# Kernel tuning notes

Measured on AMD Instinct MI355X. Metric: run time of the kernel, lower is better.

## Reference

```python
import jax, jax.numpy as jnp
import numpy as np


def setup_inputs() -> dict:
    key = jax.random.key(0)
    k1, k2, k3 = jax.random.split(key, 3)
    B, S, dk = 8, 4096, 64  # per-head tensors; dk = embedding_size / h = 1024 / 16
    q = jax.random.normal(k1, (B, S, dk), dtype=jnp.float32)
    k = jax.random.normal(k2, (B, S, dk), dtype=jnp.float32)
    v = jax.random.normal(k3, (B, S, dk), dtype=jnp.float32)
    return {"q": q, "k": k, "v": v}


def reference(q, k, v):
    dk = q.shape[-1]
    # QK = q @ k^T scaled by 1/dk (NOT 1/sqrt(dk) -- faithful to source)
    scores = jnp.einsum("bqd,bkd->bqk", q, k) / dk  # [B, S, S]
    # padding mask derived from exact-zero score entries: -inf where QK == 0
    pad_mask = jnp.where(scores == 0, -jnp.inf, 0.0)
    # look-ahead (causal) mask: 0 where i >= j else -inf
    S = scores.shape[-1]
    causal = jnp.where(
        jnp.arange(S)[:, None] >= jnp.arange(S)[None, :], 0.0, -jnp.inf
    )  # [S, S]
    scores = scores + pad_mask + causal
    attn = jax.nn.softmax(scores, axis=-1)
    # NaN cleanup for fully-masked rows (softmax over all -inf)
    attn = jnp.where(jnp.isnan(attn), 0.0, attn)
    return jnp.einsum("bqk,bkd->bqd", attn, v)
```

## Files before the change

kernel.cpp:

```cpp
#include <hip/hip_runtime.h>
#include <hip/hip_bf16.h>
#include <stdint.h>

#define S_LEN 4096
#define DK    64
#define BQ    64
#define BK    64

typedef __bf16 bf16x8  __attribute__((ext_vector_type(8)));
typedef float  f32x16  __attribute__((ext_vector_type(16)));

__device__ __forceinline__ short f2bf(float f) {
    union { __bf16 h; short s; } u; u.h = (__bf16)f; return u.s;
}
__device__ __forceinline__ short4 cvt4(float4 f) {
    short4 s; s.x = f2bf(f.x); s.y = f2bf(f.y); s.z = f2bf(f.z); s.w = f2bf(f.w); return s;
}

__device__ __forceinline__ uint32_t cvtpk_bf16(float lo, float hi) {
    uint32_t d;
    asm("v_cvt_pk_bf16_f32 %0, %1, %2" : "=&v"(d) : "v"(lo), "v"(hi));
    return d;
}
__device__ __forceinline__ void plswap(uint32_t& a, uint32_t& b) {
    asm("v_permlane32_swap_b32 %0, %1" : "+v"(a), "+v"(b));
}

__device__ __forceinline__ void gload_lds16(const void* g, void* l) {
    auto gp = reinterpret_cast<const uint32_t __attribute__((address_space(1)))*>(
        reinterpret_cast<uintptr_t>(g));
    auto lp = reinterpret_cast<uint32_t __attribute__((address_space(3)))*>(
        reinterpret_cast<uintptr_t>(l));
    __builtin_amdgcn_global_load_lds(gp, lp, 16, 0, 0);
}

__device__ __forceinline__ int swz(int row) {
    return ((row ^ (row >> 3)) & 7) << 3;
}

__global__ __launch_bounds__(256) void prep_kernel(
    const float* __restrict__ K, const float* __restrict__ V,
    short* __restrict__ WK, short* __restrict__ WV)
{
    const int t = blockIdx.x, b = blockIdx.y;
    const int tid = threadIdx.x;
    const size_t ibase = ((size_t)b * S_LEN + (size_t)t * 64) * DK;
    const size_t obase = ((size_t)b * 64 + t) * 4096;
    const int r0 = tid >> 4;
    const int c0 = (tid & 15) * 4;

    #pragma unroll
    for (int i = 0; i < 4; ++i) {
        const int row = r0 + 16 * i;
        const float4 f = *reinterpret_cast<const float4*>(K + ibase + (size_t)row * DK + c0);
        *reinterpret_cast<short4*>(WK + obase + row * 64 + (c0 ^ swz(row))) = cvt4(f);
    }
    float4 vf[4];
    #pragma unroll
    for (int j = 0; j < 4; ++j)
        vf[j] = *reinterpret_cast<const float4*>(V + ibase + (size_t)(4 * r0 + j) * DK + c0);
    #pragma unroll
    for (int jj = 0; jj < 4; ++jj) {
        const int d = c0 + jj;
        short4 sp;
        sp.x = f2bf(reinterpret_cast<const float*>(&vf[0])[jj]);
        sp.y = f2bf(reinterpret_cast<const float*>(&vf[1])[jj]);
        sp.z = f2bf(reinterpret_cast<const float*>(&vf[2])[jj]);
        sp.w = f2bf(reinterpret_cast<const float*>(&vf[3])[jj]);
        *reinterpret_cast<short4*>(WV + obase + d * 64 + ((4 * r0) ^ swz(d))) = sp;
    }
}

__global__ __launch_bounds__(512, 2) void attn_kernel(
    const float* __restrict__ Q, float* __restrict__ O,
    const short* __restrict__ WK, const short* __restrict__ WV)
{
    __shared__ __align__(16) short Ks[2][16384];
    __shared__ __align__(16) short Vts[2][16384];
    __shared__ float2 Ml[4][2][32];

    const int tid  = threadIdx.x;
    const int wave = tid >> 6;
    const int lane = tid & 63;
    const int q32  = lane & 31;
    const int hi   = lane >> 5;
    const int hi4  = hi * 4;
    const int hi8  = hi * 8;
    const int grp  = wave & 3;
    const int qsub = wave >> 2;

    const int batch = blockIdx.y;
    const size_t bo = (size_t)batch * S_LEN * DK;
    const short* WKb = WK + (size_t)batch * 262144;
    const short* WVb = WV + (size_t)batch * 262144;

    auto stage_quad = [&](int quad, int buf) {
        const char* gk = (const char*)(WKb + (size_t)quad * 16384) + wave * 1024 + lane * 16;
        const char* gv = (const char*)(WVb + (size_t)quad * 16384) + wave * 1024 + lane * 16;
        char* lk = (char*)(&Ks[buf][0]) + wave * 1024;
        char* lv = (char*)(&Vts[buf][0]) + wave * 1024;
        #pragma unroll
        for (int i = 0; i < 4; ++i) {
            gload_lds16(gk + i * 8192, lk + i * 8192);
            gload_lds16(gv + i * 8192, lv + i * 8192);
        }
    };

    const float NEG_INF = -__builtin_inff();
    const float QSCALE  = 0.015625f * 1.44269504088896341f;
    const float THR     = 8.0f;
    const int swz0 = swz(q32);
    const int swz1 = swz(32 + q32);

    #pragma unroll 1
    for (int qi = 0; qi < 2; ++qi) {
        const int qb = qi ? (int)blockIdx.x : 63 - (int)blockIdx.x;
        const int q0 = qb * BQ;
        const int ntiles = qb + 1;
        const int nquads = (ntiles + 3) >> 2;
        const int qrow   = q0 + 32 * qsub + q32;

        bf16x8 qf[4];
        {
            const float* Qr = Q + bo + (size_t)qrow * DK;
            #pragma unroll
            for (int s = 0; s < 4; ++s) {
                const float4 a = *reinterpret_cast<const float4*>(Qr + 16 * s + hi8);
                const float4 b = *reinterpret_cast<const float4*>(Qr + 16 * s + hi8 + 4);
                qf[s][0] = (__bf16)(a.x * QSCALE); qf[s][1] = (__bf16)(a.y * QSCALE);
                qf[s][2] = (__bf16)(a.z * QSCALE); qf[s][3] = (__bf16)(a.w * QSCALE);
                qf[s][4] = (__bf16)(b.x * QSCALE); qf[s][5] = (__bf16)(b.y * QSCALE);
                qf[s][6] = (__bf16)(b.z * QSCALE); qf[s][7] = (__bf16)(b.w * QSCALE);
            }
        }

        float m_run = NEG_INF, l_run = 0.f;
        f32x16 oa0, oa1;
        #pragma unroll
        for (int r = 0; r < 16; ++r) { oa0[r] = 0.f; oa1[r] = 0.f; }

        stage_quad(0, 0);
        __syncthreads();

        for (int p = 0; p < nquads; ++p) {
            const int kt = 4 * p + grp;
            const bool pf = (p + 1 < nquads);
            if (pf) stage_quad(p + 1, (p + 1) & 1);

            const short* Kt = &Ks[p & 1][grp * 4096];
            const short* Vt = &Vts[p & 1][grp * 4096];
            const bool act = (kt < ntiles);

            if (act) {
                f32x16 sa0, sa1;
                #pragma unroll
                for (int r = 0; r < 16; ++r) { sa0[r] = 0.f; sa1[r] = 0.f; }
                __builtin_amdgcn_s_setprio(1);
                #pragma unroll
                for (int s = 0; s < 4; ++s) {
                    const int col = 16 * s + hi8;
                    const bf16x8 kf0 = *reinterpret_cast<const bf16x8*>(&Kt[q32 * 64 + (col ^ swz0)]);
                    const bf16x8 kf1 = *reinterpret_cast<const bf16x8*>(&Kt[(32 + q32) * 64 + (col ^ swz1)]);
                    sa0 = __builtin_amdgcn_mfma_f32_32x32x16_bf16(kf0, qf[s], sa0, 0, 0, 0);
                    sa1 = __builtin_amdgcn_mfma_f32_32x32x16_bf16(kf1, qf[s], sa1, 0, 0, 0);
                }
                __builtin_amdgcn_s_setprio(0);

                float ma[4] = {NEG_INF, NEG_INF, NEG_INF, NEG_INF};
                if (kt == qb) {
                    const int keybase = kt * BK + hi4;
                    #pragma unroll
                    for (int r = 0; r < 16; ++r) {
                        const int kl = (r & 3) + 8 * (r >> 2);
                        if (keybase + kl > qrow) sa0[r] = NEG_INF;
                        ma[r & 3] = fmaxf(ma[r & 3], sa0[r]);
                        if (keybase + kl + 32 > qrow) sa1[r] = NEG_INF;
                        ma[r & 3] = fmaxf(ma[r & 3], sa1[r]);
                    }
                } else {
                    #pragma unroll
                    for (int r = 0; r < 16; ++r) {
                        ma[r & 3] = fmaxf(ma[r & 3], sa0[r]);
                        ma[r & 3] = fmaxf(ma[r & 3], sa1[r]);
                    }
                }
                float mt = fmaxf(fmaxf(ma[0], ma[1]), fmaxf(ma[2], ma[3]));
                mt = fmaxf(mt, __shfl_xor(mt, 32));

                if (!__all(mt <= m_run + THR)) {
                    const float mnew = fmaxf(m_run, mt);
                    const float alpha = __builtin_amdgcn_exp2f(m_run - mnew);
                    m_run = mnew;
                    l_run *= alpha;
                    #pragma unroll
                    for (int r = 0; r < 16; ++r) {
                        const float ar = __shfl(alpha, (r & 3) + 8 * (r >> 2) + hi4);
                        oa0[r] *= ar; oa1[r] *= ar;
                    }
                }

                float pp[4] = {0.f, 0.f, 0.f, 0.f};
                #pragma unroll
                for (int r = 0; r < 16; ++r) {
                    sa0[r] = __builtin_amdgcn_exp2f(sa0[r] - m_run); pp[r & 3] += sa0[r];
                    sa1[r] = __builtin_amdgcn_exp2f(sa1[r] - m_run); pp[r & 3] += sa1[r];
                }
                float ps = (pp[0] + pp[1]) + (pp[2] + pp[3]);
                ps += __shfl_xor(ps, 32);
                l_run += ps;

                __builtin_amdgcn_s_setprio(1);
                #pragma unroll
                for (int c = 0; c < 2; ++c) {
                    const f32x16& sp = c ? sa1 : sa0;
                    #pragma unroll
                    for (int s2 = 0; s2 < 2; ++s2) {
                        uint32_t a0 = cvtpk_bf16(sp[8*s2+0], sp[8*s2+1]);
                        uint32_t a1 = cvtpk_bf16(sp[8*s2+2], sp[8*s2+3]);
                        uint32_t b0 = cvtpk_bf16(sp[8*s2+4], sp[8*s2+5]);
                        uint32_t b1 = cvtpk_bf16(sp[8*s2+6], sp[8*s2+7]);
                        plswap(a0, b0);
                        plswap(a1, b1);
                        union { uint32_t u[4]; bf16x8 v; } pw;
                        pw.u[0] = a0; pw.u[1] = a1; pw.u[2] = b0; pw.u[3] = b1;
                        const int vcol = 32 * c + 16 * s2 + hi8;
                        const bf16x8 vf0 = *reinterpret_cast<const bf16x8*>(&Vt[q32 * 64 + (vcol ^ swz0)]);
                        const bf16x8 vf1 = *reinterpret_cast<const bf16x8*>(&Vt[(32 + q32) * 64 + (vcol ^ swz1)]);
                        oa0 = __builtin_amdgcn_mfma_f32_32x32x16_bf16(pw.v, vf0, oa0, 0, 0, 0);
                        oa1 = __builtin_amdgcn_mfma_f32_32x32x16_bf16(pw.v, vf1, oa1, 0, 0, 0);
                    }
                }
                __builtin_amdgcn_s_setprio(0);
            }

            __syncthreads();
        }

        if (hi == 0) Ml[grp][qsub][q32] = make_float2(m_run, l_run);
        float4* Om4 = reinterpret_cast<float4*>(&Ks[0][0]);
        if (grp != 0) {
            const int midx = (grp - 1) * 2 + qsub;
            #pragma unroll
            for (int c = 0; c < 2; ++c)
                #pragma unroll
                for (int rq = 0; rq < 4; ++rq) {
                    float4 ov;
                    if (c == 0) { ov.x = oa0[4*rq]; ov.y = oa0[4*rq+1]; ov.z = oa0[4*rq+2]; ov.w = oa0[4*rq+3]; }
                    else        { ov.x = oa1[4*rq]; ov.y = oa1[4*rq+1]; ov.z = oa1[4*rq+2]; ov.w = oa1[4*rq+3]; }
                    Om4[(midx * 8 + c * 4 + rq) * 64 + lane] = ov;
                }
        }
        __syncthreads();
        if (grp == 0) {
            const float* Omf = reinterpret_cast<const float*>(&Ks[0][0]);
            float* Ob = O + bo;
            #pragma unroll
            for (int r = 0; r < 16; ++r) {
                const int row_r = (r & 3) + 8 * (r >> 2) + hi4;
                float mg[4], lg[4];
                #pragma unroll
                for (int g = 0; g < 4; ++g) {
                    const float2 v = Ml[g][qsub][row_r];
                    mg[g] = v.x; lg[g] = v.y;
                }
                const float mtot = fmaxf(fmaxf(mg[0], mg[1]), fmaxf(mg[2], mg[3]));
                float eg[4], ltot = 0.f;
                #pragma unroll
                for (int g = 0; g < 4; ++g) {
                    eg[g] = (mg[g] == NEG_INF) ? 0.f : __builtin_amdgcn_exp2f(mg[g] - mtot);
                    ltot += eg[g] * lg[g];
                }
                const float inv = (ltot > 0.f) ? (1.0f / ltot) : 0.f;
                #pragma unroll
                for (int c = 0; c < 2; ++c) {
                    float acc = eg[0] * ((c == 0) ? oa0[r] : oa1[r]);
                    #pragma unroll
                    for (int g = 1; g < 4; ++g) {
                        const int midx = (g - 1) * 2 + qsub;
                        acc += eg[g] * Omf[((midx * 8 + c * 4 + (r >> 2)) * 64 + lane) * 4 + (r & 3)];
                    }
                    Ob[(size_t)(q0 + 32 * qsub + row_r) * DK + 32 * c + q32] = acc * inv;
                }
            }
        }
        __syncthreads();
    }
}

extern "C" void kernel_launch(void* const* d_in, const int* in_sizes, int n_in,
                              void* d_out, int out_size, void* d_ws, size_t ws_size,
                              hipStream_t stream) {
    (void)in_sizes; (void)n_in; (void)out_size; (void)ws_size;
    const float* q = (const float*)d_in[0];
    const float* k = (const float*)d_in[1];
    const float* v = (const float*)d_in[2];
    float* o = (float*)d_out;
    short* wk = (short*)d_ws;
    short* wv = wk + (size_t)8 * 64 * 4096;

    hipLaunchKernelGGL(prep_kernel, dim3(64, 8), dim3(256), 0, stream, k, v, wk, wv);
    hipLaunchKernelGGL(attn_kernel, dim3(32, 8), dim3(512), 0, stream, q, o, wk, wv);
}
```

Measured before the change: 53.37 us.

## Replace LDS-staged split-K attention with single-wave blocks reading fragments from global

The attention kernel becomes one 64-thread wave per 32 query rows. Each wave walks every causal key tile itself, loading K/V MFMA fragments straight from global memory in a new fragment-major layout written by the prep kernel. This removes LDS staging, the barriers and the cross-wave softmax merge, and launches 1024 small blocks. In exchange K/V reuse across waves now relies on the L2 cache instead of LDS. Per-wave work is no longer balanced across the causal triangle, and global-load latency is exposed without a software pipeline.

Measured after the change: 71.10 us. 1.33x slower.

```diff
diff --git a/kernel.cpp b/kernel.cpp
--- a/kernel.cpp
+++ b/kernel.cpp
@@ -4,17 +4,12 @@
 
 #define S_LEN 4096
 #define DK    64
-#define BQ    64
-#define BK    64
 
 typedef __bf16 bf16x8  __attribute__((ext_vector_type(8)));
 typedef float  f32x16  __attribute__((ext_vector_type(16)));
 
 __device__ __forceinline__ short f2bf(float f) {
     union { __bf16 h; short s; } u; u.h = (__bf16)f; return u.s;
-}
-__device__ __forceinline__ short4 cvt4(float4 f) {
-    short4 s; s.x = f2bf(f.x); s.y = f2bf(f.y); s.z = f2bf(f.z); s.w = f2bf(f.w); return s;
 }
 
 __device__ __forceinline__ uint32_t cvtpk_bf16(float lo, float hi) {
@@ -24,18 +19,6 @@
 }
 __device__ __forceinline__ void plswap(uint32_t& a, uint32_t& b) {
     asm("v_permlane32_swap_b32 %0, %1" : "+v"(a), "+v"(b));
-}
-
-__device__ __forceinline__ void gload_lds16(const void* g, void* l) {
-    auto gp = reinterpret_cast<const uint32_t __attribute__((address_space(1)))*>(
-        reinterpret_cast<uintptr_t>(g));
-    auto lp = reinterpret_cast<uint32_t __attribute__((address_space(3)))*>(
-        reinterpret_cast<uintptr_t>(l));
-    __builtin_amdgcn_global_load_lds(gp, lp, 16, 0, 0);
-}
-
-__device__ __forceinline__ int swz(int row) {
-    return ((row ^ (row >> 3)) & 7) << 3;
 }
 
 __global__ __launch_bounds__(256) void prep_kernel(
@@ -49,241 +32,180 @@
     const int r0 = tid >> 4;
     const int c0 = (tid & 15) * 4;
 
-    #pragma unroll
-    for (int i = 0; i < 4; ++i) {
-        const int row = r0 + 16 * i;
-        const float4 f = *reinterpret_cast<const float4*>(K + ibase + (size_t)row * DK + c0);
-        *reinterpret_cast<short4*>(WK + obase + row * 64 + (c0 ^ swz(row))) = cvt4(f);
-    }
-    float4 vf[4];
-    #pragma unroll
-    for (int j = 0; j < 4; ++j)
-        vf[j] = *reinterpret_cast<const float4*>(V + ibase + (size_t)(4 * r0 + j) * DK + c0);
-    #pragma unroll
-    for (int jj = 0; jj < 4; ++jj) {
-        const int d = c0 + jj;
-        short4 sp;
-        sp.x = f2bf(reinterpret_cast<const float*>(&vf[0])[jj]);
-        sp.y = f2bf(reinterpret_cast<const float*>(&vf[1])[jj]);
-        sp.z = f2bf(reinterpret_cast<const float*>(&vf[2])[jj]);
-        sp.w = f2bf(reinterpret_cast<const float*>(&vf[3])[jj]);
-        *reinterpret_cast<short4*>(WV + obase + d * 64 + ((4 * r0) ^ swz(d))) = sp;
-    }
-}
-
-__global__ __launch_bounds__(512, 2) void attn_kernel(
+    {
+        const int s = c0 >> 4, h = (c0 >> 3) & 1, e = c0 & 7;
+        #pragma unroll
+        for (int i = 0; i < 4; ++i) {
+            const int row = r0 + 16 * i;
+            const float4 f = *reinterpret_cast<const float4*>(K + ibase + (size_t)row * DK + c0);
+            short4 sp;
+            sp.x = f2bf(f.x); sp.y = f2bf(f.y); sp.z = f2bf(f.z); sp.w = f2bf(f.w);
+            *reinterpret_cast<short4*>(WK + obase + (size_t)s * 1024 + (row * 2 + h) * 8 + e) = sp;
+        }
+    }
+    {
+        float4 vf[4];
+        #pragma unroll
+        for (int j = 0; j < 4; ++j)
+            vf[j] = *reinterpret_cast<const float4*>(V + ibase + (size_t)(4 * r0 + j) * DK + c0);
+        const int sk = r0 >> 2, hk = (r0 >> 1) & 1, ek = (r0 & 1) * 4;
+        #pragma unroll
+        for (int jj = 0; jj < 4; ++jj) {
+            const int d = c0 + jj;
+            short4 sp;
+            sp.x = f2bf(reinterpret_cast<const float*>(&vf[0])[jj]);
+            sp.y = f2bf(reinterpret_cast<const float*>(&vf[1])[jj]);
+            sp.z = f2bf(reinterpret_cast<const float*>(&vf[2])[jj]);
+            sp.w = f2bf(reinterpret_cast<const float*>(&vf[3])[jj]);
+            *reinterpret_cast<short4*>(WV + obase + (size_t)sk * 1024 + (d * 2 + hk) * 8 + ek) = sp;
+        }
+    }
+}
+
+__global__ __launch_bounds__(64, 2) void attn_kernel(
     const float* __restrict__ Q, float* __restrict__ O,
     const short* __restrict__ WK, const short* __restrict__ WV)
 {
-    __shared__ __align__(16) short Ks[2][16384];
-    __shared__ __align__(16) short Vts[2][16384];
-    __shared__ float2 Ml[4][2][32];
-
-    const int tid  = threadIdx.x;
-    const int wave = tid >> 6;
-    const int lane = tid & 63;
+    const int lane = threadIdx.x;
     const int q32  = lane & 31;
     const int hi   = lane >> 5;
     const int hi4  = hi * 4;
     const int hi8  = hi * 8;
-    const int grp  = wave & 3;
-    const int qsub = wave >> 2;
 
     const int batch = blockIdx.y;
+    const int qb    = 63 - ((int)blockIdx.x >> 1);
+    const int qsub  = blockIdx.x & 1;
     const size_t bo = (size_t)batch * S_LEN * DK;
     const short* WKb = WK + (size_t)batch * 262144;
     const short* WVb = WV + (size_t)batch * 262144;
 
-    auto stage_quad = [&](int quad, int buf) {
-        const char* gk = (const char*)(WKb + (size_t)quad * 16384) + wave * 1024 + lane * 16;
-        const char* gv = (const char*)(WVb + (size_t)quad * 16384) + wave * 1024 + lane * 16;
-        char* lk = (char*)(&Ks[buf][0]) + wave * 1024;
-        char* lv = (char*)(&Vts[buf][0]) + wave * 1024;
-        #pragma unroll
-        for (int i = 0; i < 4; ++i) {
-            gload_lds16(gk + i * 8192, lk + i * 8192);
-            gload_lds16(gv + i * 8192, lv + i * 8192);
-        }
-    };
+    const int q0   = qb * 64;
+    const int qrow = q0 + 32 * qsub + q32;
+    const int idx8 = (q32 * 2 + hi) * 8;
 
     const float NEG_INF = -__builtin_inff();
+    const float MFLOOR  = -1e38f;
     const float QSCALE  = 0.015625f * 1.44269504088896341f;
     const float THR     = 8.0f;
-    const int swz0 = swz(q32);
-    const int swz1 = swz(32 + q32);
-
-    #pragma unroll 1
-    for (int qi = 0; qi < 2; ++qi) {
-        const int qb = qi ? (int)blockIdx.x : 63 - (int)blockIdx.x;
-        const int q0 = qb * BQ;
-        const int ntiles = qb + 1;
-        const int nquads = (ntiles + 3) >> 2;
-        const int qrow   = q0 + 32 * qsub + q32;
-
-        bf16x8 qf[4];
-        {
-            const float* Qr = Q + bo + (size_t)qrow * DK;
-            #pragma unroll
-            for (int s = 0; s < 4; ++s) {
-                const float4 a = *reinterpret_cast<const float4*>(Qr + 16 * s + hi8);
-                const float4 b = *reinterpret_cast<const float4*>(Qr + 16 * s + hi8 + 4);
-                qf[s][0] = (__bf16)(a.x * QSCALE); qf[s][1] = (__bf16)(a.y * QSCALE);
-                qf[s][2] = (__bf16)(a.z * QSCALE); qf[s][3] = (__bf16)(a.w * QSCALE);
-                qf[s][4] = (__bf16)(b.x * QSCALE); qf[s][5] = (__bf16)(b.y * QSCALE);
-                qf[s][6] = (__bf16)(b.z * QSCALE); qf[s][7] = (__bf16)(b.w * QSCALE);
-            }
-        }
-
-        float m_run = NEG_INF, l_run = 0.f;
-        f32x16 oa0, oa1;
-        #pragma unroll
-        for (int r = 0; r < 16; ++r) { oa0[r] = 0.f; oa1[r] = 0.f; }
-
-        stage_quad(0, 0);
-        __syncthreads();
-
-        for (int p = 0; p < nquads; ++p) {
-            const int kt = 4 * p + grp;
-            const bool pf = (p + 1 < nquads);
-            if (pf) stage_quad(p + 1, (p + 1) & 1);
-
-            const short* Kt = &Ks[p & 1][grp * 4096];
-            const short* Vt = &Vts[p & 1][grp * 4096];
-            const bool act = (kt < ntiles);
-
-            if (act) {
-                f32x16 sa0, sa1;
-                #pragma unroll
-                for (int r = 0; r < 16; ++r) { sa0[r] = 0.f; sa1[r] = 0.f; }
-                __builtin_amdgcn_s_setprio(1);
-                #pragma unroll
-                for (int s = 0; s < 4; ++s) {
-                    const int col = 16 * s + hi8;
-                    const bf16x8 kf0 = *reinterpret_cast<const bf16x8*>(&Kt[q32 * 64 + (col ^ swz0)]);
-                    const bf16x8 kf1 = *reinterpret_cast<const bf16x8*>(&Kt[(32 + q32) * 64 + (col ^ swz1)]);
-                    sa0 = __builtin_amdgcn_mfma_f32_32x32x16_bf16(kf0, qf[s], sa0, 0, 0, 0);
-                    sa1 = __builtin_amdgcn_mfma_f32_32x32x16_bf16(kf1, qf[s], sa1, 0, 0, 0);
-                }
-                __builtin_amdgcn_s_setprio(0);
-
-                float ma[4] = {NEG_INF, NEG_INF, NEG_INF, NEG_INF};
-                if (kt == qb) {
-                    const int keybase = kt * BK + hi4;
-                    #pragma unroll
-                    for (int r = 0; r < 16; ++r) {
-                        const int kl = (r & 3) + 8 * (r >> 2);
-                        if (keybase + kl > qrow) sa0[r] = NEG_INF;
-                        ma[r & 3] = fmaxf(ma[r & 3], sa0[r]);
-                        if (keybase + kl + 32 > qrow) sa1[r] = NEG_INF;
-                        ma[r & 3] = fmaxf(ma[r & 3], sa1[r]);
-                    }
-                } else {
-                    #pragma unroll
-                    for (int r = 0; r < 16; ++r) {
-                        ma[r & 3] = fmaxf(ma[r & 3], sa0[r]);
-                        ma[r & 3] = fmaxf(ma[r & 3], sa1[r]);
-                    }
-                }
-                float mt = fmaxf(fmaxf(ma[0], ma[1]), fmaxf(ma[2], ma[3]));
-                mt = fmaxf(mt, __shfl_xor(mt, 32));
-
-                if (!__all(mt <= m_run + THR)) {
-                    const float mnew = fmaxf(m_run, mt);
-                    const float alpha = __builtin_amdgcn_exp2f(m_run - mnew);
-                    m_run = mnew;
-                    l_run *= alpha;
-                    #pragma unroll
-                    for (int r = 0; r < 16; ++r) {
-                        const float ar = __shfl(alpha, (r & 3) + 8 * (r >> 2) + hi4);
-                        oa0[r] *= ar; oa1[r] *= ar;
-                    }
-                }
-
-                float pp[4] = {0.f, 0.f, 0.f, 0.f};
-                #pragma unroll
-                for (int r = 0; r < 16; ++r) {
-                    sa0[r] = __builtin_amdgcn_exp2f(sa0[r] - m_run); pp[r & 3] += sa0[r];
-                    sa1[r] = __builtin_amdgcn_exp2f(sa1[r] - m_run); pp[r & 3] += sa1[r];
-                }
-                float ps = (pp[0] + pp[1]) + (pp[2] + pp[3]);
-                ps += __shfl_xor(ps, 32);
-                l_run += ps;
-
-                __builtin_amdgcn_s_setprio(1);
-                #pragma unroll
-                for (int c = 0; c < 2; ++c) {
-                    const f32x16& sp = c ? sa1 : sa0;
-                    #pragma unroll
-                    for (int s2 = 0; s2 < 2; ++s2) {
-                        uint32_t a0 = cvtpk_bf16(sp[8*s2+0], sp[8*s2+1]);
-                        uint32_t a1 = cvtpk_bf16(sp[8*s2+2], sp[8*s2+3]);
-                        uint32_t b0 = cvtpk_bf16(sp[8*s2+4], sp[8*s2+5]);
-                        uint32_t b1 = cvtpk_bf16(sp[8*s2+6], sp[8*s2+7]);
-                        plswap(a0, b0);
-                        plswap(a1, b1);
-                        union { uint32_t u[4]; bf16x8 v; } pw;
-                        pw.u[0] = a0; pw.u[1] = a1; pw.u[2] = b0; pw.u[3] = b1;
-                        const int vcol = 32 * c + 16 * s2 + hi8;
-                        const bf16x8 vf0 = *reinterpret_cast<const bf16x8*>(&Vt[q32 * 64 + (vcol ^ swz0)]);
-                        const bf16x8 vf1 = *reinterpret_cast<const bf16x8*>(&Vt[(32 + q32) * 64 + (vcol ^ swz1)]);
-                        oa0 = __builtin_amdgcn_mfma_f32_32x32x16_bf16(pw.v, vf0, oa0, 0, 0, 0);
-                        oa1 = __builtin_amdgcn_mfma_f32_32x32x16_bf16(pw.v, vf1, oa1, 0, 0, 0);
-                    }
-                }
-                __builtin_amdgcn_s_setprio(0);
-            }
-
-            __syncthreads();
-        }
-
-        if (hi == 0) Ml[grp][qsub][q32] = make_float2(m_run, l_run);
-        float4* Om4 = reinterpret_cast<float4*>(&Ks[0][0]);
-        if (grp != 0) {
-            const int midx = (grp - 1) * 2 + qsub;
-            #pragma unroll
-            for (int c = 0; c < 2; ++c)
-                #pragma unroll
-                for (int rq = 0; rq < 4; ++rq) {
-                    float4 ov;
-                    if (c == 0) { ov.x = oa0[4*rq]; ov.y = oa0[4*rq+1]; ov.z = oa0[4*rq+2]; ov.w = oa0[4*rq+3]; }
-                    else        { ov.x = oa1[4*rq]; ov.y = oa1[4*rq+1]; ov.z = oa1[4*rq+2]; ov.w = oa1[4*rq+3]; }
-                    Om4[(midx * 8 + c * 4 + rq) * 64 + lane] = ov;
-                }
-        }
-        __syncthreads();
-        if (grp == 0) {
-            const float* Omf = reinterpret_cast<const float*>(&Ks[0][0]);
-            float* Ob = O + bo;
+
+    bf16x8 qf[4];
+    {
+        const float* Qr = Q + bo + (size_t)qrow * DK;
+        #pragma unroll
+        for (int s = 0; s < 4; ++s) {
+            const float4 a = *reinterpret_cast<const float4*>(Qr + 16 * s + hi8);
+            const float4 b = *reinterpret_cast<const float4*>(Qr + 16 * s + hi8 + 4);
+            qf[s][0] = (__bf16)(a.x * QSCALE); qf[s][1] = (__bf16)(a.y * QSCALE);
+            qf[s][2] = (__bf16)(a.z * QSCALE); qf[s][3] = (__bf16)(a.w * QSCALE);
+            qf[s][4] = (__bf16)(b.x * QSCALE); qf[s][5] = (__bf16)(b.y * QSCALE);
+            qf[s][6] = (__bf16)(b.z * QSCALE); qf[s][7] = (__bf16)(b.w * QSCALE);
+        }
+    }
+
+    float m_run = MFLOOR, l_run = 0.f;
+    f32x16 oa0, oa1;
+    #pragma unroll
+    for (int r = 0; r < 16; ++r) { oa0[r] = 0.f; oa1[r] = 0.f; }
+
+    for (int kt = 0; kt <= qb; ++kt) {
+        const short* Kt = WKb + (size_t)kt * 4096;
+        const short* Vt = WVb + (size_t)kt * 4096;
+
+        bf16x8 kf0[4], kf1[4], vf0[4], vf1[4];
+        #pragma unroll
+        for (int s = 0; s < 4; ++s) {
+            kf0[s] = *reinterpret_cast<const bf16x8*>(Kt + s * 1024 + idx8);
+            kf1[s] = *reinterpret_cast<const bf16x8*>(Kt + s * 1024 + 512 + idx8);
+        }
+        #pragma unroll
+        for (int s = 0; s < 4; ++s) {
+            vf0[s] = *reinterpret_cast<const bf16x8*>(Vt + s * 1024 + idx8);
+            vf1[s] = *reinterpret_cast<const bf16x8*>(Vt + s * 1024 + 512 + idx8);
+        }
+
+        f32x16 sa0, sa1;
+        #pragma unroll
+        for (int r = 0; r < 16; ++r) { sa0[r] = 0.f; sa1[r] = 0.f; }
+        __builtin_amdgcn_s_setprio(1);
+        #pragma unroll
+        for (int s = 0; s < 4; ++s) {
+            sa0 = __builtin_amdgcn_mfma_f32_32x32x16_bf16(kf0[s], qf[s], sa0, 0, 0, 0);
+            sa1 = __builtin_amdgcn_mfma_f32_32x32x16_bf16(kf1[s], qf[s], sa1, 0, 0, 0);
+        }
+        __builtin_amdgcn_s_setprio(0);
+
+        float ma[4] = {NEG_INF, NEG_INF, NEG_INF, NEG_INF};
+        if (kt == qb) {
+            const int keybase = kt * 64 + hi4;
             #pragma unroll
             for (int r = 0; r < 16; ++r) {
-                const int row_r = (r & 3) + 8 * (r >> 2) + hi4;
-                float mg[4], lg[4];
-                #pragma unroll
-                for (int g = 0; g < 4; ++g) {
-                    const float2 v = Ml[g][qsub][row_r];
-                    mg[g] = v.x; lg[g] = v.y;
-                }
-                const float mtot = fmaxf(fmaxf(mg[0], mg[1]), fmaxf(mg[2], mg[3]));
-                float eg[4], ltot = 0.f;
-                #pragma unroll
-                for (int g = 0; g < 4; ++g) {
-                    eg[g] = (mg[g] == NEG_INF) ? 0.f : __builtin_amdgcn_exp2f(mg[g] - mtot);
-                    ltot += eg[g] * lg[g];
-                }
-                const float inv = (ltot > 0.f) ? (1.0f / ltot) : 0.f;
-                #pragma unroll
-                for (int c = 0; c < 2; ++c) {
-                    float acc = eg[0] * ((c == 0) ? oa0[r] : oa1[r]);
-                    #pragma unroll
-                    for (int g = 1; g < 4; ++g) {
-                        const int midx = (g - 1) * 2 + qsub;
-                        acc += eg[g] * Omf[((midx * 8 + c * 4 + (r >> 2)) * 64 + lane) * 4 + (r & 3)];
-                    }
-                    Ob[(size_t)(q0 + 32 * qsub + row_r) * DK + 32 * c + q32] = acc * inv;
-                }
-            }
-        }
-        __syncthreads();
+                const int kl = (r & 3) + 8 * (r >> 2);
+                if (keybase + kl > qrow) sa0[r] = NEG_INF;
+                ma[r & 3] = fmaxf(ma[r & 3], sa0[r]);
+                if (keybase + kl + 32 > qrow) sa1[r] = NEG_INF;
+                ma[r & 3] = fmaxf(ma[r & 3], sa1[r]);
+            }
+        } else {
+            #pragma unroll
+            for (int r = 0; r < 16; ++r) {
+                ma[r & 3] = fmaxf(ma[r & 3], sa0[r]);
+                ma[r & 3] = fmaxf(ma[r & 3], sa1[r]);
+            }
+        }
+        float mt = fmaxf(fmaxf(ma[0], ma[1]), fmaxf(ma[2], ma[3]));
+        mt = fmaxf(mt, __shfl_xor(mt, 32));
+
+        if (!__all(mt <= m_run + THR)) {
+            const float mnew = fmaxf(m_run, mt);
+            const float alpha = __builtin_amdgcn_exp2f(m_run - mnew);
+            m_run = mnew;
+            l_run *= alpha;
+            #pragma unroll
+            for (int r = 0; r < 16; ++r) {
+                const float ar = __shfl(alpha, (r & 3) + 8 * (r >> 2) + hi4);
+                oa0[r] *= ar; oa1[r] *= ar;
+            }
+        }
+
+        float pp[4] = {0.f, 0.f, 0.f, 0.f};
+        #pragma unroll
+        for (int r = 0; r < 16; ++r) {
+            sa0[r] = __builtin_amdgcn_exp2f(sa0[r] - m_run); pp[r & 3] += sa0[r];
+            sa1[r] = __builtin_amdgcn_exp2f(sa1[r] - m_run); pp[r & 3] += sa1[r];
+        }
+        float ps = (pp[0] + pp[1]) + (pp[2] + pp[3]);
+        ps += __shfl_xor(ps, 32);
+        l_run += ps;
+
+        __builtin_amdgcn_s_setprio(1);
+        #pragma unroll
+        for (int c = 0; c < 2; ++c) {
+            const f32x16& sp = c ? sa1 : sa0;
+            #pragma unroll
+            for (int s2 = 0; s2 < 2; ++s2) {
+                uint32_t a0 = cvtpk_bf16(sp[8*s2+0], sp[8*s2+1]);
+                uint32_t a1 = cvtpk_bf16(sp[8*s2+2], sp[8*s2+3]);
+                uint32_t b0 = cvtpk_bf16(sp[8*s2+4], sp[8*s2+5]);
+                uint32_t b1 = cvtpk_bf16(sp[8*s2+6], sp[8*s2+7]);
+                plswap(a0, b0);
+                plswap(a1, b1);
+                union { uint32_t u[4]; bf16x8 v; } pw;
+                pw.u[0] = a0; pw.u[1] = a1; pw.u[2] = b0; pw.u[3] = b1;
+                oa0 = __builtin_amdgcn_mfma_f32_32x32x16_bf16(pw.v, vf0[2*c+s2], oa0, 0, 0, 0);
+                oa1 = __builtin_amdgcn_mfma_f32_32x32x16_bf16(pw.v, vf1[2*c+s2], oa1, 0, 0, 0);
+            }
+        }
+        __builtin_amdgcn_s_setprio(0);
+    }
+
+    const float inv = (l_run > 0.f) ? (1.0f / l_run) : 0.f;
+    float* Ob = O + bo + (size_t)(q0 + 32 * qsub) * DK;
+    #pragma unroll
+    for (int r = 0; r < 16; ++r) {
+        const int row = (r & 3) + 8 * (r >> 2) + hi4;
+        const float ir = __shfl(inv, row);
+        Ob[(size_t)row * DK + q32]      = oa0[r] * ir;
+        Ob[(size_t)row * DK + 32 + q32] = oa1[r] * ir;
     }
 }
 
@@ -299,5 +221,5 @@
     short* wv = wk + (size_t)8 * 64 * 4096;
 
     hipLaunchKernelGGL(prep_kernel, dim3(64, 8), dim3(256), 0, stream, k, v, wk, wv);
-    hipLaunchKernelGGL(attn_kernel, dim3(32, 8), dim3(512), 0, stream, q, o, wk, wv);
-}
+    hipLaunchKernelGGL(attn_kernel, dim3(128, 8), dim3(64), 0, stream, q, o, wk, wv);
+}
```
